# Kernel optimization log

Hardware: AMD Instinct MI355X
Metric: run time of the kernel (lower is better)

## Reference

```python
import jax, jax.numpy as jnp
import numpy as np

SPATIAL = ((100, 134), (50, 67), (25, 34), (13, 17))
LEN = sum(h * w for h, w in SPATIAL)   # 17821
D, H, L, P = 384, 8, 4, 4
DH = D // H                            # 48
U = D // 3                             # unit_dim = 128
EPS = 1e-5


def _ln(x, g, b):
    m = jnp.mean(x, -1, keepdims=True)
    v = jnp.mean((x - m) ** 2, -1, keepdims=True)
    return (x - m) * jax.lax.rsqrt(v + EPS) * g + b


def _ffn(t, w1, b1, w2, b2, g, b):
    t2 = jax.nn.relu(t @ w1.T + b1) @ w2.T + b2
    return _ln(t + t2, g, b)


def _msda_core(value, loc, attn):
    # value [B,Lv,H,DH]; loc [B,Lq,H,L,P,2] normalized to [0,1]; attn [B,Lq,H,L,P]
    B = value.shape[0]
    Lq = loc.shape[1]
    out = jnp.zeros((B, H, Lq, DH), value.dtype)
    start = 0
    for lvl, (Hl, Wl) in enumerate(SPATIAL):
        n = Hl * Wl
        v = value[:, start:start + n].transpose(0, 2, 1, 3)        # [B,H,n,DH]
        # grid_sample(align_corners=False) semantics: pixel coord = loc*W - 0.5
        x = loc[:, :, :, lvl, :, 0] * Wl - 0.5                      # [B,Lq,H,P]
        y = loc[:, :, :, lvl, :, 1] * Hl - 0.5
        x0 = jnp.floor(x); y0 = jnp.floor(y)
        dx = x - x0; dy = y - y0
        x0i = x0.astype(jnp.int32); y0i = y0.astype(jnp.int32)
        acc = jnp.zeros((B, H, Lq, P, DH), value.dtype)
        corners = ((0, 0, (1 - dx) * (1 - dy)), (1, 0, dx * (1 - dy)),
                   (0, 1, (1 - dx) * dy), (1, 1, dx * dy))
        for ox, oy, w in corners:
            xi = x0i + ox; yi = y0i + oy
            valid = ((xi >= 0) & (xi < Wl) & (yi >= 0) & (yi < Hl)).astype(value.dtype)
            idx = jnp.clip(yi, 0, Hl - 1) * Wl + jnp.clip(xi, 0, Wl - 1)
            idx_t = idx.transpose(0, 2, 1, 3).reshape(B, H, Lq * P)
            g = jnp.take_along_axis(v, idx_t[..., None], axis=2).reshape(B, H, Lq, P, DH)
            acc = acc + g * (w * valid).transpose(0, 2, 1, 3)[..., None]
        out = out + (acc * attn[:, :, :, lvl].transpose(0, 2, 1, 3)[..., None]).sum(axis=3)
        start += n
    return out.transpose(0, 2, 1, 3).reshape(B, Lq, D)


def setup_inputs() -> dict:
    key = jax.random.key(0)
    ks = jax.random.split(key, 16)
    rn = lambda k, s, sc=1.0: jax.random.normal(k, s, jnp.float32) * sc
    inp = {}
    inp['src'] = rn(ks[0], (1, LEN, D))
    inp['space_query'] = rn(ks[1], (1, 1, 2 * U))
    inp['chann_query'] = rn(ks[2], (1, 1, 2 * U))
    inp['pos'] = rn(ks[3], (1, LEN, D))
    inp['reference_points'] = jax.random.uniform(ks[4], (1, LEN, L, 2), jnp.float32)
    inp['spatial_shapes'] = jnp.array(SPATIAL, jnp.int32)
    starts = np.cumsum([0] + [h * w for h, w in SPATIAL[:-1]])
    inp['level_start_index'] = jnp.array(starts, jnp.int32)
    inp['padding_mask'] = jnp.zeros((1, LEN), bool)
    # MSDeformAttn params (torch Linear convention: W is [out_features, in_features])
    inp['W_off'] = rn(ks[5], (H * L * P * 2, D), 0.01)
    inp['b_off'] = rn(ks[6], (H * L * P * 2,), 0.1)
    inp['W_attn'] = rn(ks[7], (H * L * P, D), D ** -0.5)
    inp['b_attn'] = jnp.zeros((H * L * P,), jnp.float32)
    inp['W_val'] = rn(ks[8], (D, D), D ** -0.5)
    inp['b_val'] = jnp.zeros((D,), jnp.float32)
    inp['W_out'] = rn(ks[9], (D, D), D ** -0.5)
    inp['b_out'] = jnp.zeros((D,), jnp.float32)
    # norm1_xy / norm1_zd
    inp['g1xy'] = jnp.ones((2 * U,), jnp.float32); inp['b1xy'] = jnp.zeros((2 * U,), jnp.float32)
    inp['g1zd'] = jnp.ones((U,), jnp.float32); inp['b1zd'] = jnp.zeros((U,), jnp.float32)
    # ffn_xy: Linear(2U,2U) -> relu -> Linear(2U,2U), residual + LN
    inp['fxy_w1'] = rn(ks[10], (2 * U, 2 * U), (2 * U) ** -0.5); inp['fxy_b1'] = jnp.zeros((2 * U,), jnp.float32)
    inp['fxy_w2'] = rn(ks[11], (2 * U, 2 * U), (2 * U) ** -0.5); inp['fxy_b2'] = jnp.zeros((2 * U,), jnp.float32)
    inp['fxy_g'] = jnp.ones((2 * U,), jnp.float32); inp['fxy_b'] = jnp.zeros((2 * U,), jnp.float32)
    # ffn_zd: Linear(U,U) -> relu -> Linear(U,U), residual + LN
    inp['fzd_w1'] = rn(ks[12], (U, U), U ** -0.5); inp['fzd_b1'] = jnp.zeros((U,), jnp.float32)
    inp['fzd_w2'] = rn(ks[13], (U, U), U ** -0.5); inp['fzd_b2'] = jnp.zeros((U,), jnp.float32)
    inp['fzd_g'] = jnp.ones((U,), jnp.float32); inp['fzd_b'] = jnp.zeros((U,), jnp.float32)
    return inp


def reference(src, space_query, chann_query, pos, reference_points, spatial_shapes,
              level_start_index, padding_mask,
              W_off, b_off, W_attn, b_attn, W_val, b_val, W_out, b_out,
              g1xy, b1xy, g1zd, b1zd,
              fxy_w1, fxy_b1, fxy_w2, fxy_b2, fxy_g, fxy_b,
              fzd_w1, fzd_b1, fzd_w2, fzd_b2, fzd_g, fzd_b):
    B, Lq, _ = src.shape
    q = src + pos                                        # with_pos_embed
    value = src @ W_val.T + b_val
    value = jnp.where(padding_mask[..., None], 0.0, value).reshape(B, Lq, H, DH)
    off = (q @ W_off.T + b_off).reshape(B, Lq, H, L, P, 2)
    attn = jax.nn.softmax((q @ W_attn.T + b_attn).reshape(B, Lq, H, L * P), -1)
    attn = attn.reshape(B, Lq, H, L, P)
    wh = jnp.array([[w, h] for h, w in SPATIAL], src.dtype)         # [L,2] as (W,H)
    loc = reference_points[:, :, None, :, None, :] + off / wh[None, None, None, :, None, :]
    src2 = _msda_core(value, loc, attn) @ W_out.T + b_out
    src_xy = _ln(src[..., :2 * U] + src2[..., :2 * U], g1xy, b1xy)
    src_zd = _ln(src[..., 2 * U:] + src2[..., 2 * U:], g1zd, b1zd)
    src_xy = _ffn(src_xy, fxy_w1, fxy_b1, fxy_w2, fxy_b2, fxy_g, fxy_b)
    src_zd = _ffn(src_zd, fzd_w1, fzd_b1, fzd_w2, fzd_b2, fzd_g, fzd_b)
    return jnp.concatenate([src_xy, src_zd], axis=-1)
```

## Files before the change

kernel.cpp:

```cpp
#include <hip/hip_runtime.h>
#include <math.h>

#define LEN 17821
#define DMODEL 384
#define NHEAD 8
#define DHEAD 48
#define WSZ (384 * 384)

typedef float floatx4 __attribute__((ext_vector_type(4)));
typedef float floatx2 __attribute__((ext_vector_type(2)));
typedef short shortx8 __attribute__((ext_vector_type(8)));
typedef unsigned short ushort;

__device__ inline ushort f2bf(float f) {
    unsigned int u = __float_as_uint(f);
    u += 0x7FFFu + ((u >> 16) & 1u);
    return (ushort)(u >> 16);
}
__device__ inline float bf2f(ushort s) {
    return __uint_as_float(((unsigned int)s) << 16);
}

__device__ inline floatx4 mfma_bf16(shortx8 a, shortx8 b, floatx4 c) {
    return __builtin_amdgcn_mfma_f32_16x16x32_bf16(a, b, c, 0, 0, 0);
}

__global__ __launch_bounds__(256)
void prep_w(const float* __restrict__ Wval, const float* __restrict__ Woff,
            const float* __restrict__ Wattn, const float* __restrict__ Wout,
            const float* __restrict__ w1xy, const float* __restrict__ w1zd,
            const float* __restrict__ w2xy, const float* __restrict__ w2zd,
            ushort* __restrict__ wv, ushort* __restrict__ woa,
            ushort* __restrict__ wo, ushort* __restrict__ w1b,
            ushort* __restrict__ w2b) {
    int idx = blockIdx.x * 256 + threadIdx.x;
    if (idx >= WSZ) return;
    int job = blockIdx.y;
    float v; ushort* dst;
    if (job <= 1) {
        int n = idx / 384, k = idx - n * 384;
        if (job == 0) { v = Wval[idx]; dst = wv; }
        else {
            v = n < 256 ? Woff[n * 384 + k] : Wattn[(n - 256) * 384 + k];
            dst = woa;
        }
    } else {
        int e = idx & 7;
        int lane = (idx >> 3) & 63;
        int t = idx >> 9;
        int j = t % 3;
        int t2 = t / 3;
        int wv8 = t2 & 7;
        int hs = t2 >> 3;
        int l15 = lane & 15, quad = lane >> 4;
        int row = wv8 * 48 + j * 16 + l15;
        int k = hs * 32 + quad * 8 + e;
        if (job == 2) { v = Wout[row * 384 + k]; dst = wo; }
        else if (job == 3) {
            v = row < 256 ? (k < 256 ? w1xy[row * 256 + k] : 0.f)
                          : (k >= 256 ? w1zd[(row - 256) * 128 + (k - 256)] : 0.f);
            dst = w1b;
        } else {
            v = row < 256 ? (k < 256 ? w2xy[row * 256 + k] : 0.f)
                          : (k >= 256 ? w2zd[(row - 256) * 128 + (k - 256)] : 0.f);
            dst = w2b;
        }
    }
    dst[idx] = f2bf(v);
}

__global__ __launch_bounds__(384)
void prep_b(const float* __restrict__ boff, const float* __restrict__ battn,
            const float* __restrict__ b1xy, const float* __restrict__ b1zd,
            const float* __restrict__ b2xy, const float* __restrict__ b2zd,
            const float* __restrict__ g1xy, const float* __restrict__ be1xy,
            const float* __restrict__ g1zd, const float* __restrict__ be1zd,
            const float* __restrict__ g2xy, const float* __restrict__ be2xy,
            const float* __restrict__ g2zd, const float* __restrict__ be2zd,
            float* __restrict__ boa, float* __restrict__ b1c,
            float* __restrict__ b2c, float* __restrict__ l1g,
            float* __restrict__ l1b, float* __restrict__ l2g,
            float* __restrict__ l2b) {
    int i = threadIdx.x;
    bool lo = i < 256; int j = lo ? i : i - 256;
    boa[i] = lo ? boff[i] : battn[j];
    b1c[i] = lo ? b1xy[i] : b1zd[j];
    b2c[i] = lo ? b2xy[i] : b2zd[j];
    l1g[i] = lo ? g1xy[i] : g1zd[j];
    l1b[i] = lo ? be1xy[i] : be1zd[j];
    l2g[i] = lo ? g2xy[i] : g2zd[j];
    l2b[i] = lo ? be2xy[i] : be2zd[j];
}

__global__ __launch_bounds__(256)
void cvt_add(const float* __restrict__ src, const float* __restrict__ pos,
             ushort* __restrict__ src_bf, ushort* __restrict__ q_bf, int n8) {
    int i = blockIdx.x * 256 + threadIdx.x;
    if (i >= n8) return;
    float4 s0 = ((const float4*)src)[i * 2], s1 = ((const float4*)src)[i * 2 + 1];
    float4 p0 = ((const float4*)pos)[i * 2], p1 = ((const float4*)pos)[i * 2 + 1];
    shortx8 sb, qb;
    sb[0] = f2bf(s0.x); sb[1] = f2bf(s0.y); sb[2] = f2bf(s0.z); sb[3] = f2bf(s0.w);
    sb[4] = f2bf(s1.x); sb[5] = f2bf(s1.y); sb[6] = f2bf(s1.z); sb[7] = f2bf(s1.w);
    qb[0] = f2bf(s0.x + p0.x); qb[1] = f2bf(s0.y + p0.y);
    qb[2] = f2bf(s0.z + p0.z); qb[3] = f2bf(s0.w + p0.w);
    qb[4] = f2bf(s1.x + p1.x); qb[5] = f2bf(s1.y + p1.y);
    qb[6] = f2bf(s1.z + p1.z); qb[7] = f2bf(s1.w + p1.w);
    ((shortx8*)src_bf)[i] = sb;
    ((shortx8*)q_bf)[i] = qb;
}

#define TSV 128
#define LSTRIDE 40

__global__ __launch_bounds__(256)
void vq_gemm(const ushort* __restrict__ sbq, const ushort* __restrict__ qbq,
             const ushort* __restrict__ wv, const ushort* __restrict__ woa,
             const float* __restrict__ bval, const float* __restrict__ boa,
             ushort* __restrict__ vout, float* __restrict__ oaout) {
    __shared__ ushort As[TSV * LSTRIDE];
    __shared__ ushort Ws[TSV * LSTRIDE];
    bool job = blockIdx.x >= 3;
    int bx = job ? blockIdx.x - 3 : blockIdx.x;
    const ushort* A = job ? qbq : sbq;
    const ushort* W = job ? woa : wv;
    const float* bias = job ? boa : bval;
    int tid = threadIdx.x;
    int lane = tid & 63, wave = tid >> 6;
    int wr = (wave >> 1) * 64, wc = (wave & 1) * 64;
    int l15 = lane & 15, quad = lane >> 4;
    int srow = tid >> 1, shalf = tid & 1;
    int by = blockIdx.y;
    int garow = by * TSV + srow;
    bool avalid = garow < LEN;
    const ushort* ap = A + (size_t)(avalid ? garow : 0) * 384 + shalf * 16;
    const ushort* wp = W + (size_t)(bx * TSV + srow) * 384 + shalf * 16;
    ushort* as_dst = &As[srow * LSTRIDE + shalf * 16];
    ushort* ws_dst = &Ws[srow * LSTRIDE + shalf * 16];

    floatx4 acc[4][4];
    #pragma unroll
    for (int i = 0; i < 4; ++i)
        #pragma unroll
        for (int j = 0; j < 4; ++j)
            acc[i][j] = (floatx4){0.f, 0.f, 0.f, 0.f};

    shortx8 a0 = *(const shortx8*)(ap);
    shortx8 a1 = *(const shortx8*)(ap + 8);
    shortx8 w0 = *(const shortx8*)(wp);
    shortx8 w1 = *(const shortx8*)(wp + 8);

    for (int k0 = 0; k0 < 384; k0 += 32) {
        __syncthreads();
        *(shortx8*)(as_dst + 0) = a0;
        *(shortx8*)(as_dst + 8) = a1;
        *(shortx8*)(ws_dst + 0) = w0;
        *(shortx8*)(ws_dst + 8) = w1;
        __syncthreads();
        if (k0 + 32 < 384) {
            a0 = *(const shortx8*)(ap + k0 + 32);
            a1 = *(const shortx8*)(ap + k0 + 40);
            w0 = *(const shortx8*)(wp + k0 + 32);
            w1 = *(const shortx8*)(wp + k0 + 40);
        }
        shortx8 af[4], bfr[4];
        #pragma unroll
        for (int i = 0; i < 4; ++i)
            af[i] = *(shortx8*)&As[(wr + i * 16 + l15) * LSTRIDE + quad * 8];
        #pragma unroll
        for (int j = 0; j < 4; ++j)
            bfr[j] = *(shortx8*)&Ws[(wc + j * 16 + l15) * LSTRIDE + quad * 8];
        #pragma unroll
        for (int i = 0; i < 4; ++i)
            #pragma unroll
            for (int j = 0; j < 4; ++j)
                acc[i][j] = __builtin_amdgcn_mfma_f32_16x16x32_bf16(
                    af[i], bfr[j], acc[i][j], 0, 0, 0);
    }

    #pragma unroll
    for (int j = 0; j < 4; ++j) {
        int col = bx * TSV + wc + j * 16 + l15;
        float bv = bias[col];
        #pragma unroll
        for (int i = 0; i < 4; ++i) {
            #pragma unroll
            for (int r = 0; r < 4; ++r) {
                int row = by * TSV + wr + i * 16 + quad * 4 + r;
                if (row < LEN) {
                    float v = acc[i][j][r] + bv;
                    if (job) oaout[(size_t)row * 384 + col] = v;
                    else     vout[(size_t)row * 384 + col] = f2bf(v);
                }
            }
        }
    }
}

#define MTOK 8
#define NXCD 8
__global__ __launch_bounds__(384)
void msda_v4(const ushort* __restrict__ value,
             const float* __restrict__ offattn,
             const float* __restrict__ refpts,
             ushort* __restrict__ out, int nwg) {
    __shared__ float saw[MTOK * 128];
    __shared__ int   si4[MTOK * 128][4];
    __shared__ float sw4[MTOK * 128][4];
    constexpr int Wi[4]  = {134, 67, 34, 17};
    constexpr int Hi[4]  = {100, 50, 25, 13};
    constexpr int STi[4] = {0, 13400, 16750, 17600};

    int orig = blockIdx.x;
    int q = nwg / NXCD, r = nwg % NXCD;
    int xcd = orig % NXCD, ci = orig / NXCD;
    int bid = (xcd < r ? xcd * (q + 1) : r * (q + 1) + (xcd - r) * q) + ci;
    int t0 = bid * MTOK;
    int tid = threadIdx.x;

    if (tid < MTOK * 8) {
        int ti = tid >> 3, h = tid & 7, t = t0 + ti;
        if (t < LEN) {
            const float* lg = offattn + (size_t)t * 384 + 256 + h * 16;
            float w[16], mx = -3.4e38f;
            #pragma unroll
            for (int s = 0; s < 16; ++s) { w[s] = lg[s]; mx = fmaxf(mx, w[s]); }
            float sum = 0.f;
            #pragma unroll
            for (int s = 0; s < 16; ++s) { w[s] = __expf(w[s] - mx); sum += w[s]; }
            float inv = 1.0f / sum;
            #pragma unroll
            for (int s = 0; s < 16; ++s) saw[ti * 128 + h * 16 + s] = w[s] * inv;
        }
    }
    __syncthreads();

    for (int idx = tid; idx < MTOK * 128; idx += 384) {
        int ti = idx >> 7, rem = idx & 127, h = rem >> 4, p = rem & 15;
        int lvl = p >> 2, pp = p & 3;
        int t = t0 + ti;
        if (t < LEN) {
            float Wl = (float)Wi[lvl], Hl = (float)Hi[lvl];
            const int Wli = Wi[lvl], Hli = Hi[lvl], st = STi[lvl];
            const float* op = offattn + (size_t)t * 384 + h * 32 + lvl * 8 + pp * 2;
            float ox = op[0], oy = op[1];
            float rx = refpts[(size_t)t * 8 + lvl * 2];
            float ry = refpts[(size_t)t * 8 + lvl * 2 + 1];
            float x = rx * Wl + ox - 0.5f;
            float y = ry * Hl + oy - 0.5f;
            float x0f = floorf(x), y0f = floorf(y);
            int x0 = (int)x0f, y0 = (int)y0f;
            float dx = x - x0f, dy = y - y0f;
            float aw = saw[idx];
            float cwv[4] = {(1.f - dx) * (1.f - dy), dx * (1.f - dy),
                            (1.f - dx) * dy, dx * dy};
            #pragma unroll
            for (int c2 = 0; c2 < 4; ++c2) {
                int xi = x0 + (c2 & 1), yi = y0 + (c2 >> 1);
                bool valid = (xi >= 0) & (xi < Wli) & (yi >= 0) & (yi < Hli);
                int xc = min(max(xi, 0), Wli - 1);
                int yc = min(max(yi, 0), Hli - 1);
                si4[idx][c2] = st + yc * Wli + xc;
                sw4[idx][c2] = valid ? aw * cwv[c2] : 0.f;
            }
        }
    }
    __syncthreads();

    int ti = tid / 48;
    int rr = tid - ti * 48;
    int h = rr / 6;
    int c = rr - h * 6;
    int t = t0 + ti;
    if (t >= LEN) return;
    const ushort* vb = value + h * DHEAD + c * 8;
    floatx2 a2[4] = {};
    #pragma unroll
    for (int p = 0; p < 16; ++p) {
        int base = ti * 128 + h * 16 + p;
        int4  I = *(const int4*)&si4[base][0];
        float4 W4 = *(const float4*)&sw4[base][0];
        const int   Iv[4] = {I.x, I.y, I.z, I.w};
        const float Wv[4] = {W4.x, W4.y, W4.z, W4.w};
        #pragma unroll
        for (int c2 = 0; c2 < 4; ++c2) {
            shortx8 g = *(const shortx8*)(vb + (size_t)Iv[c2] * 384);
            float s = Wv[c2];
            floatx2 s2 = {s, s};
            const unsigned int* gu = (const unsigned int*)&g;
            #pragma unroll
            for (int q2 = 0; q2 < 4; ++q2) {
                unsigned int u = gu[q2];
                floatx2 gf;
                gf[0] = __uint_as_float(u << 16);
                gf[1] = __uint_as_float(u & 0xFFFF0000u);
                a2[q2] += s2 * gf;
            }
        }
    }
    shortx8 o;
    #pragma unroll
    for (int q2 = 0; q2 < 4; ++q2) {
        o[q2 * 2]     = f2bf(a2[q2][0]);
        o[q2 * 2 + 1] = f2bf(a2[q2][1]);
    }
    *(shortx8*)(out + (size_t)t * 384 + h * DHEAD + c * 8) = o;
}

#define MT 32
#define CST 392

#define GEMM384(WPTR)                                                         \
  {                                                                           \
    const ushort* wp_ = (WPTR) + wave * 1536 + lane * 8;                      \
    _Pragma("unroll")                                                         \
    for (int i_ = 0; i_ < 2; ++i_)                                            \
      _Pragma("unroll")                                                       \
      for (int j_ = 0; j_ < 3; ++j_) acc[i_][j_] = (floatx4){0.f,0.f,0.f,0.f};\
    shortx8 wcr[3], wnr[3];                                                   \
    _Pragma("unroll")                                                         \
    for (int j_ = 0; j_ < 3; ++j_)                                            \
      wcr[j_] = *(const shortx8*)(wp_ + j_ * 512);                            \
    _Pragma("unroll")                                                         \
    for (int hs = 0; hs < 12; ++hs) {                                         \
      if (hs < 11) {                                                          \
        _Pragma("unroll")                                                     \
        for (int j_ = 0; j_ < 3; ++j_)                                        \
          wnr[j_] = *(const shortx8*)(wp_ + (hs + 1) * 12288 + j_ * 512);     \
      }                                                                       \
      shortx8 a0 = *(shortx8*)&Cbuf[l15 * CST + hs * 32 + quad * 8];          \
      shortx8 a1 = *(shortx8*)&Cbuf[(16 + l15) * CST + hs * 32 + quad * 8];   \
      _Pragma("unroll")                                                       \
      for (int j_ = 0; j_ < 3; ++j_) {                                        \
        acc[0][j_] = mfma_bf16(a0, wcr[j_], acc[0][j_]);                      \
        acc[1][j_] = mfma_bf16(a1, wcr[j_], acc[1][j_]);                      \
      }                                                                       \
      if (hs < 11) {                                                          \
        _Pragma("unroll")                                                     \
        for (int j_ = 0; j_ < 3; ++j_) wcr[j_] = wnr[j_];                     \
      }                                                                       \
    }                                                                         \
  }

__global__ __launch_bounds__(512, 2)
void mega_kernel(const ushort* __restrict__ Amsda, const float* __restrict__ src,
                 const ushort* __restrict__ Wo, const ushort* __restrict__ W1,
                 const ushort* __restrict__ W2,
                 const float* __restrict__ bo, const float* __restrict__ b1c,
                 const float* __restrict__ b2c,
                 const float* __restrict__ l1g, const float* __restrict__ l1b,
                 const float* __restrict__ l2g, const float* __restrict__ l2b,
                 float* __restrict__ h1f, float* __restrict__ outp) {
    __shared__ __align__(16) ushort Cbuf[MT * CST];
    __shared__ __align__(16) floatx4 pst4[MT * 16];
    __shared__ __align__(16) floatx4 lnf[MT];

    int tid = threadIdx.x;
    int lane = tid & 63, wave = tid >> 6;
    int l15 = lane & 15, quad = lane >> 4;
    int wcol = wave * 48;
    int by0 = blockIdx.x * MT;

    floatx4 acc[2][3];

    #pragma unroll
    for (int cix = 0; cix < 3; ++cix) {
        int idx = cix * 512 + tid;
        int row = idx / 48, c = idx - row * 48;
        int gr = min(by0 + row, LEN - 1);
        *(shortx8*)(Cbuf + row * CST + c * 8) =
            *(const shortx8*)(Amsda + (size_t)gr * 384 + c * 8);
    }
    __syncthreads();

    GEMM384(Wo);
    __syncthreads();

    #pragma unroll
    for (int j = 0; j < 3; ++j) {
        int col = wcol + j * 16 + l15;
        float bv = bo[col];
        #pragma unroll
        for (int i = 0; i < 2; ++i)
            #pragma unroll
            for (int rr = 0; rr < 4; ++rr) {
                int row = i * 16 + quad * 4 + rr;
                int gr = min(by0 + row, LEN - 1);
                float x = acc[i][j][rr] + bv + src[(size_t)gr * 384 + col];
                Cbuf[row * CST + col] = f2bf(x);
            }
    }
    __syncthreads();

    {
        int row = tid >> 4, part = tid & 15;
        float sx = 0.f, qx = 0.f, sz = 0.f, qz = 0.f;
        #pragma unroll
        for (int m = 0; m < 3; ++m) {
            int c0 = part * 24 + m * 8;
            shortx8 v = *(shortx8*)(Cbuf + row * CST + c0);
            float cs = 0.f, cq = 0.f;
            #pragma unroll
            for (int e = 0; e < 8; ++e) { float x = bf2f(v[e]); cs += x; cq += x * x; }
            if (c0 < 256) { sx += cs; qx += cq; } else { sz += cs; qz += cq; }
        }
        pst4[row * 16 + part] = (floatx4){sx, qx, sz, qz};
    }
    __syncthreads();
    if (tid < MT) {
        floatx4 s = (floatx4){0.f, 0.f, 0.f, 0.f};
        #pragma unroll
        for (int p = 0; p < 16; ++p) s += pst4[tid * 16 + p];
        float mx = s[0] / 256.f, vx = s[1] / 256.f - mx * mx;
        float mz = s[2] / 128.f, vz = s[3] / 128.f - mz * mz;
        lnf[tid] = (floatx4){mx, rsqrtf(vx + 1e-5f), mz, rsqrtf(vz + 1e-5f)};
    }
    __syncthreads();
    {
        int row = tid >> 4, part = tid & 15;
        int gr = by0 + row;
        floatx4 L = lnf[row];
        #pragma unroll
        for (int m = 0; m < 3; ++m) {
            int c0 = part * 24 + m * 8;
            bool isxy = c0 < 256;
            float mean = isxy ? L[0] : L[2];
            float inv  = isxy ? L[1] : L[3];
            shortx8 v = *(shortx8*)(Cbuf + row * CST + c0);
            float4 g0 = *(const float4*)(l1g + c0), g1 = *(const float4*)(l1g + c0 + 4);
            float4 e0 = *(const float4*)(l1b + c0), e1 = *(const float4*)(l1b + c0 + 4);
            float gg[8] = {g0.x, g0.y, g0.z, g0.w, g1.x, g1.y, g1.z, g1.w};
            float ee[8] = {e0.x, e0.y, e0.z, e0.w, e1.x, e1.y, e1.z, e1.w};
            float h[8];
            shortx8 hb;
            #pragma unroll
            for (int e = 0; e < 8; ++e) {
                h[e] = (bf2f(v[e]) - mean) * inv * gg[e] + ee[e];
                hb[e] = f2bf(h[e]);
            }
            *(shortx8*)(Cbuf + row * CST + c0) = hb;
            if (gr < LEN) {
                *(float4*)(h1f + (size_t)gr * 384 + c0)     = make_float4(h[0], h[1], h[2], h[3]);
                *(float4*)(h1f + (size_t)gr * 384 + c0 + 4) = make_float4(h[4], h[5], h[6], h[7]);
            }
        }
    }
    __syncthreads();

    GEMM384(W1);
    __syncthreads();
    #pragma unroll
    for (int j = 0; j < 3; ++j) {
        int col = wcol + j * 16 + l15;
        float bv = b1c[col];
        #pragma unroll
        for (int i = 0; i < 2; ++i)
            #pragma unroll
            for (int rr = 0; rr < 4; ++rr) {
                int row = i * 16 + quad * 4 + rr;
                Cbuf[row * CST + col] = f2bf(fmaxf(acc[i][j][rr] + bv, 0.f));
            }
    }
    __syncthreads();

    GEMM384(W2);
    __syncthreads();
    #pragma unroll
    for (int j = 0; j < 3; ++j) {
        int col = wcol + j * 16 + l15;
        float bv = b2c[col];
        #pragma unroll
        for (int i = 0; i < 2; ++i)
            #pragma unroll
            for (int rr = 0; rr < 4; ++rr) {
                int row = i * 16 + quad * 4 + rr;
                int gr = min(by0 + row, LEN - 1);
                float x = acc[i][j][rr] + bv + h1f[(size_t)gr * 384 + col];
                Cbuf[row * CST + col] = f2bf(x);
            }
    }
    __syncthreads();

    {
        int row = tid >> 4, part = tid & 15;
        float sx = 0.f, qx = 0.f, sz = 0.f, qz = 0.f;
        #pragma unroll
        for (int m = 0; m < 3; ++m) {
            int c0 = part * 24 + m * 8;
            shortx8 v = *(shortx8*)(Cbuf + row * CST + c0);
            float cs = 0.f, cq = 0.f;
            #pragma unroll
            for (int e = 0; e < 8; ++e) { float x = bf2f(v[e]); cs += x; cq += x * x; }
            if (c0 < 256) { sx += cs; qx += cq; } else { sz += cs; qz += cq; }
        }
        pst4[row * 16 + part] = (floatx4){sx, qx, sz, qz};
    }
    __syncthreads();
    if (tid < MT) {
        floatx4 s = (floatx4){0.f, 0.f, 0.f, 0.f};
        #pragma unroll
        for (int p = 0; p < 16; ++p) s += pst4[tid * 16 + p];
        float mx = s[0] / 256.f, vx = s[1] / 256.f - mx * mx;
        float mz = s[2] / 128.f, vz = s[3] / 128.f - mz * mz;
        lnf[tid] = (floatx4){mx, rsqrtf(vx + 1e-5f), mz, rsqrtf(vz + 1e-5f)};
    }
    __syncthreads();
    {
        int row = tid >> 4, part = tid & 15;
        int gr = by0 + row;
        if (gr < LEN) {
            floatx4 L = lnf[row];
            #pragma unroll
            for (int m = 0; m < 3; ++m) {
                int c0 = part * 24 + m * 8;
                bool isxy = c0 < 256;
                float mean = isxy ? L[0] : L[2];
                float inv  = isxy ? L[1] : L[3];
                shortx8 v = *(shortx8*)(Cbuf + row * CST + c0);
                float4 g0 = *(const float4*)(l2g + c0), g1 = *(const float4*)(l2g + c0 + 4);
                float4 e0 = *(const float4*)(l2b + c0), e1 = *(const float4*)(l2b + c0 + 4);
                float gg[8] = {g0.x, g0.y, g0.z, g0.w, g1.x, g1.y, g1.z, g1.w};
                float ee[8] = {e0.x, e0.y, e0.z, e0.w, e1.x, e1.y, e1.z, e1.w};
                float h[8];
                #pragma unroll
                for (int e = 0; e < 8; ++e)
                    h[e] = (bf2f(v[e]) - mean) * inv * gg[e] + ee[e];
                *(float4*)(outp + (size_t)gr * 384 + c0)     = make_float4(h[0], h[1], h[2], h[3]);
                *(float4*)(outp + (size_t)gr * 384 + c0 + 4) = make_float4(h[4], h[5], h[6], h[7]);
            }
        }
    }
}

extern "C" void kernel_launch(void* const* d_in, const int* in_sizes, int n_in,
                              void* d_out, int out_size, void* d_ws, size_t ws_size,
                              hipStream_t stream) {
    const float* src    = (const float*)d_in[0];
    const float* pos    = (const float*)d_in[3];
    const float* refpts = (const float*)d_in[4];
    const float* W_off  = (const float*)d_in[8];
    const float* b_off  = (const float*)d_in[9];
    const float* W_attn = (const float*)d_in[10];
    const float* b_attn = (const float*)d_in[11];
    const float* W_val  = (const float*)d_in[12];
    const float* b_val  = (const float*)d_in[13];
    const float* W_out  = (const float*)d_in[14];
    const float* b_out  = (const float*)d_in[15];
    const float* g1xy = (const float*)d_in[16]; const float* b1xy = (const float*)d_in[17];
    const float* g1zd = (const float*)d_in[18]; const float* b1zd = (const float*)d_in[19];
    const float* fxy_w1 = (const float*)d_in[20]; const float* fxy_b1 = (const float*)d_in[21];
    const float* fxy_w2 = (const float*)d_in[22]; const float* fxy_b2 = (const float*)d_in[23];
    const float* fxy_g  = (const float*)d_in[24]; const float* fxy_b  = (const float*)d_in[25];
    const float* fzd_w1 = (const float*)d_in[26]; const float* fzd_b1 = (const float*)d_in[27];
    const float* fzd_w2 = (const float*)d_in[28]; const float* fzd_b2 = (const float*)d_in[29];
    const float* fzd_g  = (const float*)d_in[30]; const float* fzd_b  = (const float*)d_in[31];

    float* out = (float*)d_out;
    size_t Rn = (size_t)LEN * DMODEL;

    float* f0 = (float*)d_ws;
    ushort* sb = (ushort*)(f0 + Rn);
    ushort* s0 = sb;
    ushort* s1 = sb + Rn;
    ushort* s2 = sb + 2 * Rn;
    ushort* s3 = sb + 3 * Rn;
    ushort* wv  = sb + 4 * Rn;
    ushort* woa = wv + WSZ;
    ushort* wo  = woa + WSZ;
    ushort* w1b = wo + WSZ;
    ushort* w2b = w1b + WSZ;
    float* bp = (float*)(w2b + WSZ);
    float* boa = bp;        float* b1c = bp + 384;  float* b2c = bp + 768;
    float* l1g = bp + 1152; float* l1b = bp + 1536;
    float* l2g = bp + 1920; float* l2b = bp + 2304;

    prep_w<<<dim3((WSZ + 255) / 256, 5), 256, 0, stream>>>(
        W_val, W_off, W_attn, W_out, fxy_w1, fzd_w1, fxy_w2, fzd_w2,
        wv, woa, wo, w1b, w2b);
    prep_b<<<1, 384, 0, stream>>>(b_off, b_attn, fxy_b1, fzd_b1, fxy_b2, fzd_b2,
                                  g1xy, b1xy, g1zd, b1zd, fxy_g, fxy_b, fzd_g, fzd_b,
                                  boa, b1c, b2c, l1g, l1b, l2g, l2b);

    int n8 = (int)(Rn / 8);
    cvt_add<<<(n8 + 255) / 256, 256, 0, stream>>>(src, pos, s0, s1, n8);

    vq_gemm<<<dim3(6, (LEN + TSV - 1) / TSV), 256, 0, stream>>>(
        s0, s1, wv, woa, b_val, boa, s2, f0);

    int nwg = (LEN + MTOK - 1) / MTOK;
    msda_v4<<<nwg, 384, 0, stream>>>(s2, f0, refpts, s3, nwg);

    mega_kernel<<<(LEN + MT - 1) / MT, 512, 0, stream>>>(
        s3, src, wo, w1b, w2b, b_out, b1c, b2c,
        l1g, l1b, l2g, l2b, f0, out);
}
```

Before: 305.2 us.

## Fuse fp32-to-bf16 conversion and pos add into value/offset GEMM

```diff
diff --git a/kernel.cpp b/kernel.cpp
--- a/kernel.cpp
+++ b/kernel.cpp
@@ -36,35 +36,30 @@
     int idx = blockIdx.x * 256 + threadIdx.x;
     if (idx >= WSZ) return;
     int job = blockIdx.y;
+    int e = idx & 7;
+    int lane = (idx >> 3) & 63;
+    int t = idx >> 9;
+    int j = t % 3;
+    int t2 = t / 3;
+    int wv8 = t2 & 7;
+    int hs = t2 >> 3;
+    int l15 = lane & 15, quad = lane >> 4;
+    int row = wv8 * 48 + j * 16 + l15;
+    int k = hs * 32 + quad * 8 + e;
     float v; ushort* dst;
-    if (job <= 1) {
-        int n = idx / 384, k = idx - n * 384;
-        if (job == 0) { v = Wval[idx]; dst = wv; }
-        else {
-            v = n < 256 ? Woff[n * 384 + k] : Wattn[(n - 256) * 384 + k];
-            dst = woa;
-        }
+    if (job == 0) { v = Wval[row * 384 + k]; dst = wv; }
+    else if (job == 1) {
+        v = row < 256 ? Woff[row * 384 + k] : Wattn[(row - 256) * 384 + k];
+        dst = woa;
+    } else if (job == 2) { v = Wout[row * 384 + k]; dst = wo; }
+    else if (job == 3) {
+        v = row < 256 ? (k < 256 ? w1xy[row * 256 + k] : 0.f)
+                      : (k >= 256 ? w1zd[(row - 256) * 128 + (k - 256)] : 0.f);
+        dst = w1b;
     } else {
-        int e = idx & 7;
-        int lane = (idx >> 3) & 63;
-        int t = idx >> 9;
-        int j = t % 3;
-        int t2 = t / 3;
-        int wv8 = t2 & 7;
-        int hs = t2 >> 3;
-        int l15 = lane & 15, quad = lane >> 4;
-        int row = wv8 * 48 + j * 16 + l15;
-        int k = hs * 32 + quad * 8 + e;
-        if (job == 2) { v = Wout[row * 384 + k]; dst = wo; }
-        else if (job == 3) {
-            v = row < 256 ? (k < 256 ? w1xy[row * 256 + k] : 0.f)
-                          : (k >= 256 ? w1zd[(row - 256) * 128 + (k - 256)] : 0.f);
-            dst = w1b;
-        } else {
-            v = row < 256 ? (k < 256 ? w2xy[row * 256 + k] : 0.f)
-                          : (k >= 256 ? w2zd[(row - 256) * 128 + (k - 256)] : 0.f);
-            dst = w2b;
-        }
+        v = row < 256 ? (k < 256 ? w2xy[row * 256 + k] : 0.f)
+                      : (k >= 256 ? w2zd[(row - 256) * 128 + (k - 256)] : 0.f);
+        dst = w2b;
     }
     dst[idx] = f2bf(v);
 }
@@ -90,221 +85,6 @@
     l1b[i] = lo ? be1xy[i] : be1zd[j];
     l2g[i] = lo ? g2xy[i] : g2zd[j];
     l2b[i] = lo ? be2xy[i] : be2zd[j];
-}
-
-__global__ __launch_bounds__(256)
-void cvt_add(const float* __restrict__ src, const float* __restrict__ pos,
-             ushort* __restrict__ src_bf, ushort* __restrict__ q_bf, int n8) {
-    int i = blockIdx.x * 256 + threadIdx.x;
-    if (i >= n8) return;
-    float4 s0 = ((const float4*)src)[i * 2], s1 = ((const float4*)src)[i * 2 + 1];
-    float4 p0 = ((const float4*)pos)[i * 2], p1 = ((const float4*)pos)[i * 2 + 1];
-    shortx8 sb, qb;
-    sb[0] = f2bf(s0.x); sb[1] = f2bf(s0.y); sb[2] = f2bf(s0.z); sb[3] = f2bf(s0.w);
-    sb[4] = f2bf(s1.x); sb[5] = f2bf(s1.y); sb[6] = f2bf(s1.z); sb[7] = f2bf(s1.w);
-    qb[0] = f2bf(s0.x + p0.x); qb[1] = f2bf(s0.y + p0.y);
-    qb[2] = f2bf(s0.z + p0.z); qb[3] = f2bf(s0.w + p0.w);
-    qb[4] = f2bf(s1.x + p1.x); qb[5] = f2bf(s1.y + p1.y);
-    qb[6] = f2bf(s1.z + p1.z); qb[7] = f2bf(s1.w + p1.w);
-    ((shortx8*)src_bf)[i] = sb;
-    ((shortx8*)q_bf)[i] = qb;
-}
-
-#define TSV 128
-#define LSTRIDE 40
-
-__global__ __launch_bounds__(256)
-void vq_gemm(const ushort* __restrict__ sbq, const ushort* __restrict__ qbq,
-             const ushort* __restrict__ wv, const ushort* __restrict__ woa,
-             const float* __restrict__ bval, const float* __restrict__ boa,
-             ushort* __restrict__ vout, float* __restrict__ oaout) {
-    __shared__ ushort As[TSV * LSTRIDE];
-    __shared__ ushort Ws[TSV * LSTRIDE];
-    bool job = blockIdx.x >= 3;
-    int bx = job ? blockIdx.x - 3 : blockIdx.x;
-    const ushort* A = job ? qbq : sbq;
-    const ushort* W = job ? woa : wv;
-    const float* bias = job ? boa : bval;
-    int tid = threadIdx.x;
-    int lane = tid & 63, wave = tid >> 6;
-    int wr = (wave >> 1) * 64, wc = (wave & 1) * 64;
-    int l15 = lane & 15, quad = lane >> 4;
-    int srow = tid >> 1, shalf = tid & 1;
-    int by = blockIdx.y;
-    int garow = by * TSV + srow;
-    bool avalid = garow < LEN;
-    const ushort* ap = A + (size_t)(avalid ? garow : 0) * 384 + shalf * 16;
-    const ushort* wp = W + (size_t)(bx * TSV + srow) * 384 + shalf * 16;
-    ushort* as_dst = &As[srow * LSTRIDE + shalf * 16];
-    ushort* ws_dst = &Ws[srow * LSTRIDE + shalf * 16];
-
-    floatx4 acc[4][4];
-    #pragma unroll
-    for (int i = 0; i < 4; ++i)
-        #pragma unroll
-        for (int j = 0; j < 4; ++j)
-            acc[i][j] = (floatx4){0.f, 0.f, 0.f, 0.f};
-
-    shortx8 a0 = *(const shortx8*)(ap);
-    shortx8 a1 = *(const shortx8*)(ap + 8);
-    shortx8 w0 = *(const shortx8*)(wp);
-    shortx8 w1 = *(const shortx8*)(wp + 8);
-
-    for (int k0 = 0; k0 < 384; k0 += 32) {
-        __syncthreads();
-        *(shortx8*)(as_dst + 0) = a0;
-        *(shortx8*)(as_dst + 8) = a1;
-        *(shortx8*)(ws_dst + 0) = w0;
-        *(shortx8*)(ws_dst + 8) = w1;
-        __syncthreads();
-        if (k0 + 32 < 384) {
-            a0 = *(const shortx8*)(ap + k0 + 32);
-            a1 = *(const shortx8*)(ap + k0 + 40);
-            w0 = *(const shortx8*)(wp + k0 + 32);
-            w1 = *(const shortx8*)(wp + k0 + 40);
-        }
-        shortx8 af[4], bfr[4];
-        #pragma unroll
-        for (int i = 0; i < 4; ++i)
-            af[i] = *(shortx8*)&As[(wr + i * 16 + l15) * LSTRIDE + quad * 8];
-        #pragma unroll
-        for (int j = 0; j < 4; ++j)
-            bfr[j] = *(shortx8*)&Ws[(wc + j * 16 + l15) * LSTRIDE + quad * 8];
-        #pragma unroll
-        for (int i = 0; i < 4; ++i)
-            #pragma unroll
-            for (int j = 0; j < 4; ++j)
-                acc[i][j] = __builtin_amdgcn_mfma_f32_16x16x32_bf16(
-                    af[i], bfr[j], acc[i][j], 0, 0, 0);
-    }
-
-    #pragma unroll
-    for (int j = 0; j < 4; ++j) {
-        int col = bx * TSV + wc + j * 16 + l15;
-        float bv = bias[col];
-        #pragma unroll
-        for (int i = 0; i < 4; ++i) {
-            #pragma unroll
-            for (int r = 0; r < 4; ++r) {
-                int row = by * TSV + wr + i * 16 + quad * 4 + r;
-                if (row < LEN) {
-                    float v = acc[i][j][r] + bv;
-                    if (job) oaout[(size_t)row * 384 + col] = v;
-                    else     vout[(size_t)row * 384 + col] = f2bf(v);
-                }
-            }
-        }
-    }
-}
-
-#define MTOK 8
-#define NXCD 8
-__global__ __launch_bounds__(384)
-void msda_v4(const ushort* __restrict__ value,
-             const float* __restrict__ offattn,
-             const float* __restrict__ refpts,
-             ushort* __restrict__ out, int nwg) {
-    __shared__ float saw[MTOK * 128];
-    __shared__ int   si4[MTOK * 128][4];
-    __shared__ float sw4[MTOK * 128][4];
-    constexpr int Wi[4]  = {134, 67, 34, 17};
-    constexpr int Hi[4]  = {100, 50, 25, 13};
-    constexpr int STi[4] = {0, 13400, 16750, 17600};
-
-    int orig = blockIdx.x;
-    int q = nwg / NXCD, r = nwg % NXCD;
-    int xcd = orig % NXCD, ci = orig / NXCD;
-    int bid = (xcd < r ? xcd * (q + 1) : r * (q + 1) + (xcd - r) * q) + ci;
-    int t0 = bid * MTOK;
-    int tid = threadIdx.x;
-
-    if (tid < MTOK * 8) {
-        int ti = tid >> 3, h = tid & 7, t = t0 + ti;
-        if (t < LEN) {
-            const float* lg = offattn + (size_t)t * 384 + 256 + h * 16;
-            float w[16], mx = -3.4e38f;
-            #pragma unroll
-            for (int s = 0; s < 16; ++s) { w[s] = lg[s]; mx = fmaxf(mx, w[s]); }
-            float sum = 0.f;
-            #pragma unroll
-            for (int s = 0; s < 16; ++s) { w[s] = __expf(w[s] - mx); sum += w[s]; }
-            float inv = 1.0f / sum;
-            #pragma unroll
-            for (int s = 0; s < 16; ++s) saw[ti * 128 + h * 16 + s] = w[s] * inv;
-        }
-    }
-    __syncthreads();
-
-    for (int idx = tid; idx < MTOK * 128; idx += 384) {
-        int ti = idx >> 7, rem = idx & 127, h = rem >> 4, p = rem & 15;
-        int lvl = p >> 2, pp = p & 3;
-        int t = t0 + ti;
-        if (t < LEN) {
-            float Wl = (float)Wi[lvl], Hl = (float)Hi[lvl];
-            const int Wli = Wi[lvl], Hli = Hi[lvl], st = STi[lvl];
-            const float* op = offattn + (size_t)t * 384 + h * 32 + lvl * 8 + pp * 2;
-            float ox = op[0], oy = op[1];
-            float rx = refpts[(size_t)t * 8 + lvl * 2];
-            float ry = refpts[(size_t)t * 8 + lvl * 2 + 1];
-            float x = rx * Wl + ox - 0.5f;
-            float y = ry * Hl + oy - 0.5f;
-            float x0f = floorf(x), y0f = floorf(y);
-            int x0 = (int)x0f, y0 = (int)y0f;
-            float dx = x - x0f, dy = y - y0f;
-            float aw = saw[idx];
-            float cwv[4] = {(1.f - dx) * (1.f - dy), dx * (1.f - dy),
-                            (1.f - dx) * dy, dx * dy};
-            #pragma unroll
-            for (int c2 = 0; c2 < 4; ++c2) {
-                int xi = x0 + (c2 & 1), yi = y0 + (c2 >> 1);
-                bool valid = (xi >= 0) & (xi < Wli) & (yi >= 0) & (yi < Hli);
-                int xc = min(max(xi, 0), Wli - 1);
-                int yc = min(max(yi, 0), Hli - 1);
-                si4[idx][c2] = st + yc * Wli + xc;
-                sw4[idx][c2] = valid ? aw * cwv[c2] : 0.f;
-            }
-        }
-    }
-    __syncthreads();
-
-    int ti = tid / 48;
-    int rr = tid - ti * 48;
-    int h = rr / 6;
-    int c = rr - h * 6;
-    int t = t0 + ti;
-    if (t >= LEN) return;
-    const ushort* vb = value + h * DHEAD + c * 8;
-    floatx2 a2[4] = {};
-    #pragma unroll
-    for (int p = 0; p < 16; ++p) {
-        int base = ti * 128 + h * 16 + p;
-        int4  I = *(const int4*)&si4[base][0];
-        float4 W4 = *(const float4*)&sw4[base][0];
-        const int   Iv[4] = {I.x, I.y, I.z, I.w};
-        const float Wv[4] = {W4.x, W4.y, W4.z, W4.w};
-        #pragma unroll
-        for (int c2 = 0; c2 < 4; ++c2) {
-            shortx8 g = *(const shortx8*)(vb + (size_t)Iv[c2] * 384);
-            float s = Wv[c2];
-            floatx2 s2 = {s, s};
-            const unsigned int* gu = (const unsigned int*)&g;
-            #pragma unroll
-            for (int q2 = 0; q2 < 4; ++q2) {
-                unsigned int u = gu[q2];
-                floatx2 gf;
-                gf[0] = __uint_as_float(u << 16);
-                gf[1] = __uint_as_float(u & 0xFFFF0000u);
-                a2[q2] += s2 * gf;
-            }
-        }
-    }
-    shortx8 o;
-    #pragma unroll
-    for (int q2 = 0; q2 < 4; ++q2) {
-        o[q2 * 2]     = f2bf(a2[q2][0]);
-        o[q2 * 2 + 1] = f2bf(a2[q2][1]);
-    }
-    *(shortx8*)(out + (size_t)t * 384 + h * DHEAD + c * 8) = o;
 }
 
 #define MT 32
@@ -343,6 +123,173 @@
   }
 
 __global__ __launch_bounds__(512, 2)
+void vq_gemm(const float* __restrict__ src, const float* __restrict__ pos,
+             const ushort* __restrict__ wv, const ushort* __restrict__ woa,
+             const float* __restrict__ bval, const float* __restrict__ boa,
+             ushort* __restrict__ vout, float* __restrict__ oaout) {
+    __shared__ __align__(16) ushort Cbuf[MT * CST];
+    bool job = blockIdx.y != 0;
+    const ushort* Wp = job ? woa : wv;
+    const float* bias = job ? boa : bval;
+    int tid = threadIdx.x;
+    int lane = tid & 63, wave = tid >> 6;
+    int l15 = lane & 15, quad = lane >> 4;
+    int wcol = wave * 48;
+    int by0 = blockIdx.x * MT;
+
+    #pragma unroll
+    for (int cix = 0; cix < 3; ++cix) {
+        int idx = cix * 512 + tid;
+        int row = idx / 48, c = idx - row * 48;
+        int gr = min(by0 + row, LEN - 1);
+        const float* sp = src + (size_t)gr * 384 + c * 8;
+        float4 a0 = *(const float4*)sp, a1 = *(const float4*)(sp + 4);
+        if (job) {
+            const float* pp = pos + (size_t)gr * 384 + c * 8;
+            float4 p0 = *(const float4*)pp, p1 = *(const float4*)(pp + 4);
+            a0.x += p0.x; a0.y += p0.y; a0.z += p0.z; a0.w += p0.w;
+            a1.x += p1.x; a1.y += p1.y; a1.z += p1.z; a1.w += p1.w;
+        }
+        shortx8 b;
+        b[0] = f2bf(a0.x); b[1] = f2bf(a0.y); b[2] = f2bf(a0.z); b[3] = f2bf(a0.w);
+        b[4] = f2bf(a1.x); b[5] = f2bf(a1.y); b[6] = f2bf(a1.z); b[7] = f2bf(a1.w);
+        *(shortx8*)(Cbuf + row * CST + c * 8) = b;
+    }
+    __syncthreads();
+
+    floatx4 acc[2][3];
+    GEMM384(Wp);
+
+    #pragma unroll
+    for (int j = 0; j < 3; ++j) {
+        int col = wcol + j * 16 + l15;
+        float bv = bias[col];
+        #pragma unroll
+        for (int i = 0; i < 2; ++i) {
+            #pragma unroll
+            for (int rr = 0; rr < 4; ++rr) {
+                int gr = by0 + i * 16 + quad * 4 + rr;
+                if (gr < LEN) {
+                    float v = acc[i][j][rr] + bv;
+                    if (job) oaout[(size_t)gr * 384 + col] = v;
+                    else     vout[(size_t)gr * 384 + col] = f2bf(v);
+                }
+            }
+        }
+    }
+}
+
+#define MTOK 8
+#define NXCD 8
+__global__ __launch_bounds__(384)
+void msda_v4(const ushort* __restrict__ value,
+             const float* __restrict__ offattn,
+             const float* __restrict__ refpts,
+             ushort* __restrict__ out, int nwg) {
+    __shared__ float saw[MTOK * 128];
+    __shared__ int   si4[MTOK * 128][4];
+    __shared__ float sw4[MTOK * 128][4];
+    constexpr int Wi[4]  = {134, 67, 34, 17};
+    constexpr int Hi[4]  = {100, 50, 25, 13};
+    constexpr int STi[4] = {0, 13400, 16750, 17600};
+
+    int orig = blockIdx.x;
+    int q = nwg / NXCD, r = nwg % NXCD;
+    int xcd = orig % NXCD, ci = orig / NXCD;
+    int bid = (xcd < r ? xcd * (q + 1) : r * (q + 1) + (xcd - r) * q) + ci;
+    int t0 = bid * MTOK;
+    int tid = threadIdx.x;
+
+    if (tid < MTOK * 8) {
+        int ti = tid >> 3, h = tid & 7, t = t0 + ti;
+        if (t < LEN) {
+            const float* lg = offattn + (size_t)t * 384 + 256 + h * 16;
+            float w[16], mx = -3.4e38f;
+            #pragma unroll
+            for (int s = 0; s < 16; ++s) { w[s] = lg[s]; mx = fmaxf(mx, w[s]); }
+            float sum = 0.f;
+            #pragma unroll
+            for (int s = 0; s < 16; ++s) { w[s] = __expf(w[s] - mx); sum += w[s]; }
+            float inv = 1.0f / sum;
+            #pragma unroll
+            for (int s = 0; s < 16; ++s) saw[ti * 128 + h * 16 + s] = w[s] * inv;
+        }
+    }
+    __syncthreads();
+
+    for (int idx = tid; idx < MTOK * 128; idx += 384) {
+        int ti = idx >> 7, rem = idx & 127, h = rem >> 4, p = rem & 15;
+        int lvl = p >> 2, pp = p & 3;
+        int t = t0 + ti;
+        if (t < LEN) {
+            float Wl = (float)Wi[lvl], Hl = (float)Hi[lvl];
+            const int Wli = Wi[lvl], Hli = Hi[lvl], st = STi[lvl];
+            const float* op = offattn + (size_t)t * 384 + h * 32 + lvl * 8 + pp * 2;
+            float ox = op[0], oy = op[1];
+            float rx = refpts[(size_t)t * 8 + lvl * 2];
+            float ry = refpts[(size_t)t * 8 + lvl * 2 + 1];
+            float x = rx * Wl + ox - 0.5f;
+            float y = ry * Hl + oy - 0.5f;
+            float x0f = floorf(x), y0f = floorf(y);
+            int x0 = (int)x0f, y0 = (int)y0f;
+            float dx = x - x0f, dy = y - y0f;
+            float aw = saw[idx];
+            float cwv[4] = {(1.f - dx) * (1.f - dy), dx * (1.f - dy),
+                            (1.f - dx) * dy, dx * dy};
+            #pragma unroll
+            for (int c2 = 0; c2 < 4; ++c2) {
+                int xi = x0 + (c2 & 1), yi = y0 + (c2 >> 1);
+                bool valid = (xi >= 0) & (xi < Wli) & (yi >= 0) & (yi < Hli);
+                int xc = min(max(xi, 0), Wli - 1);
+                int yc = min(max(yi, 0), Hli - 1);
+                si4[idx][c2] = st + yc * Wli + xc;
+                sw4[idx][c2] = valid ? aw * cwv[c2] : 0.f;
+            }
+        }
+    }
+    __syncthreads();
+
+    int ti = tid / 48;
+    int rr = tid - ti * 48;
+    int h = rr / 6;
+    int c = rr - h * 6;
+    int t = t0 + ti;
+    if (t >= LEN) return;
+    const ushort* vb = value + h * DHEAD + c * 8;
+    floatx2 a2[4] = {};
+    #pragma unroll
+    for (int p = 0; p < 16; ++p) {
+        int base = ti * 128 + h * 16 + p;
+        int4  I = *(const int4*)&si4[base][0];
+        float4 W4 = *(const float4*)&sw4[base][0];
+        const int   Iv[4] = {I.x, I.y, I.z, I.w};
+        const float Wv[4] = {W4.x, W4.y, W4.z, W4.w};
+        #pragma unroll
+        for (int c2 = 0; c2 < 4; ++c2) {
+            shortx8 g = *(const shortx8*)(vb + (size_t)Iv[c2] * 384);
+            float s = Wv[c2];
+            floatx2 s2 = {s, s};
+            const unsigned int* gu = (const unsigned int*)&g;
+            #pragma unroll
+            for (int q2 = 0; q2 < 4; ++q2) {
+                unsigned int u = gu[q2];
+                floatx2 gf;
+                gf[0] = __uint_as_float(u << 16);
+                gf[1] = __uint_as_float(u & 0xFFFF0000u);
+                a2[q2] += s2 * gf;
+            }
+        }
+    }
+    shortx8 o;
+    #pragma unroll
+    for (int q2 = 0; q2 < 4; ++q2) {
+        o[q2 * 2]     = f2bf(a2[q2][0]);
+        o[q2 * 2 + 1] = f2bf(a2[q2][1]);
+    }
+    *(shortx8*)(out + (size_t)t * 384 + h * DHEAD + c * 8) = o;
+}
+
+__global__ __launch_bounds__(512, 2)
 void mega_kernel(const ushort* __restrict__ Amsda, const float* __restrict__ src,
                  const ushort* __restrict__ Wo, const ushort* __restrict__ W1,
                  const ushort* __restrict__ W2,
@@ -560,8 +507,6 @@
 
     float* f0 = (float*)d_ws;
     ushort* sb = (ushort*)(f0 + Rn);
-    ushort* s0 = sb;
-    ushort* s1 = sb + Rn;
     ushort* s2 = sb + 2 * Rn;
     ushort* s3 = sb + 3 * Rn;
     ushort* wv  = sb + 4 * Rn;
@@ -581,11 +526,8 @@
                                   g1xy, b1xy, g1zd, b1zd, fxy_g, fxy_b, fzd_g, fzd_b,
                                   boa, b1c, b2c, l1g, l1b, l2g, l2b);
 
-    int n8 = (int)(Rn / 8);
-    cvt_add<<<(n8 + 255) / 256, 256, 0, stream>>>(src, pos, s0, s1, n8);
-
-    vq_gemm<<<dim3(6, (LEN + TSV - 1) / TSV), 256, 0, stream>>>(
-        s0, s1, wv, woa, b_val, boa, s2, f0);
+    vq_gemm<<<dim3((LEN + MT - 1) / MT, 2), 512, 0, stream>>>(
+        src, pos, wv, woa, b_val, boa, s2, f0);
 
     int nwg = (LEN + MTOK - 1) / MTOK;
     msda_v4<<<nwg, 384, 0, stream>>>(s2, f0, refpts, s3, nwg);
```

Result: faster. 296.2 us (-2.9%).
